# Kernel optimization log

Hardware: AMD Instinct MI355X
Metric: run time of the kernel (lower is better)

## Reference

```python
import jax, jax.numpy as jnp
import numpy as np

K = 3            # kernel_size
PAD = K // 2
CENTER_OFFSET = 0.0


def obb2offset(obb, stride):
    """obb: [N,5,H,W] (x_ctr,y_ctr,w,h,theta) in image coords -> deform offsets [N,2*K*K,H,W]."""
    N, _, H, W = obb.shape
    idx = jnp.arange(-PAD, PAD + 1, dtype=jnp.float32)
    yy, xx = jnp.meshgrid(idx, idx, indexing='ij')   # torch.meshgrid default 'ij'
    xx = xx.reshape(-1)                               # [KK]
    yy = yy.reshape(-1)
    x_ctr, y_ctr, w, h, a = [obb[:, i] for i in range(5)]   # each [N,H,W]
    s = jnp.float32(stride)
    x_ctr, y_ctr, w, h = x_ctr / s, y_ctr / s, w / s, h / s
    cos, sin = jnp.cos(a), jnp.sin(a)
    dw, dh = w / K, h / K
    px = dw[..., None] * xx                           # [N,H,W,KK]
    py = dh[..., None] * yy
    xr = cos[..., None] * px - sin[..., None] * py    # rotate kernel grid by theta
    yr = sin[..., None] * px + cos[..., None] * py
    x_anchor = xr + x_ctr[..., None]
    y_anchor = yr + y_ctr[..., None]
    xc = jnp.arange(W, dtype=jnp.float32)
    yc = jnp.arange(H, dtype=jnp.float32)
    x_conv = xc[None, None, :, None] + xx + CENTER_OFFSET   # [1,1,W,KK]
    y_conv = yc[None, :, None, None] + yy + CENTER_OFFSET   # [1,H,1,KK]
    off = jnp.stack([y_anchor - y_conv, x_anchor - x_conv], axis=-1)  # [N,H,W,KK,2]
    return off.reshape(N, H, W, 2 * K * K).transpose(0, 3, 1, 2)


def deform_conv(x, offsets, weight):
    """Deformable conv v1, zero padding, stride 1. x:[N,Cin,H,W], offsets:[N,2KK,H,W], weight:[Cout,Cin,K,K]."""
    N, Cin, H, W = x.shape
    KK = K * K
    Cout = weight.shape[0]
    off = offsets.reshape(N, KK, 2, H, W)
    dy, dx = off[:, :, 0], off[:, :, 1]                        # [N,KK,H,W]
    ky = jnp.arange(KK, dtype=jnp.float32) // K - PAD
    kx = jnp.arange(KK, dtype=jnp.float32) % K - PAD
    py = jnp.arange(H, dtype=jnp.float32)[None, None, :, None] + ky[None, :, None, None] + dy
    px = jnp.arange(W, dtype=jnp.float32)[None, None, None, :] + kx[None, :, None, None] + dx
    y0 = jnp.floor(py)
    x0 = jnp.floor(px)
    ly = py - y0                                               # bilinear fractions
    lx = px - x0
    y0i = y0.astype(jnp.int32)
    x0i = x0.astype(jnp.int32)
    x_flat = x.reshape(N, Cin, H * W)

    def corner(iy, ix):
        valid = (iy >= 0) & (iy < H) & (ix >= 0) & (ix < W)
        idx = jnp.clip(iy, 0, H - 1) * W + jnp.clip(ix, 0, W - 1)  # [N,KK,H,W]
        g = jax.vmap(lambda xf, ii: xf[:, ii.reshape(-1)].reshape(Cin, KK, H, W))(x_flat, idx)
        return jnp.where(valid[:, None], g, 0.0)               # [N,Cin,KK,H,W]

    v00 = corner(y0i, x0i)
    v01 = corner(y0i, x0i + 1)
    v10 = corner(y0i + 1, x0i)
    v11 = corner(y0i + 1, x0i + 1)
    wy = ly[:, None]
    wx = lx[:, None]
    sampled = (v00 * (1 - wy) * (1 - wx) + v01 * (1 - wy) * wx
               + v10 * wy * (1 - wx) + v11 * wy * wx)          # [N,Cin,KK,H,W]
    return jnp.einsum('nckhw,ock->nohw', sampled, weight.reshape(Cout, Cin, KK))


def setup_inputs() -> dict:
    key = jax.random.key(0)
    k1, k2, k3, k4, k5, k6 = jax.random.split(key, 6)
    N, Cin, Cout, H, W, stride = 2, 256, 256, 128, 128, 8
    x = jax.random.normal(k1, (N, Cin, H, W), jnp.float32)
    gy, gx = jnp.meshgrid(jnp.arange(H, dtype=jnp.float32), jnp.arange(W, dtype=jnp.float32), indexing='ij')
    xc = (gx[None] + jax.random.uniform(k2, (N, H, W), minval=-0.5, maxval=0.5)) * stride
    yc = (gy[None] + jax.random.uniform(k3, (N, H, W), minval=-0.5, maxval=0.5)) * stride
    wb = jax.random.uniform(k4, (N, H, W), minval=2.0 * stride, maxval=8.0 * stride)
    hb = jax.random.uniform(k5, (N, H, W), minval=2.0 * stride, maxval=8.0 * stride)
    th = jax.random.uniform(k6, (N, H, W), minval=-np.pi / 2, maxval=np.pi / 2)
    obb = jnp.stack([xc, yc, wb, hb, th], axis=1)              # [N,5,H,W]
    weight = jax.random.normal(jax.random.fold_in(key, 7), (Cout, Cin, K, K), jnp.float32) * 0.02
    return {"x": x, "obb": obb, "weight": weight, "stride": stride}


def reference(x, obb, weight, stride):
    offsets = obb2offset(jax.lax.stop_gradient(obb), stride)   # offsets.detach() in original
    return deform_conv(x, offsets, weight)
```

## Files before the change

### kernel.cpp

```cpp
#include <hip/hip_runtime.h>

#define HH 128
#define WW 128
#define CIN 256
#define COUT 256
#define KTOT 2304
#define HW (HH * WW)
#define NIT 36

typedef __attribute__((ext_vector_type(8))) short short8;
typedef __attribute__((ext_vector_type(4))) float f32x4;
typedef __attribute__((ext_vector_type(2))) float f32x2;

__device__ __forceinline__ unsigned rne_bf16(float f) {
  unsigned u = __float_as_uint(f);
  return (u + 0x7FFFu + ((u >> 16) & 1u)) >> 16;
}
__device__ __forceinline__ unsigned cvt_pk_bf16(float lo, float hi) {
  unsigned r;
  asm("v_cvt_pk_bf16_f32 %0, %1, %2" : "=v"(r) : "v"(lo), "v"(hi));
  return r;
}
__device__ __forceinline__ f32x2 up2(unsigned u) {
  f32x2 r;
  r.x = __uint_as_float(u << 16);
  r.y = __uint_as_float(u & 0xFFFF0000u);
  return r;
}
__device__ __forceinline__ f32x2 pkmul(f32x2 w, f32x2 v) {
  f32x2 d;
  asm("v_pk_mul_f32 %0, %1, %2" : "=v"(d) : "v"(w), "v"(v));
  return d;
}
__device__ __forceinline__ f32x2 pkfma(f32x2 w, f32x2 v, f32x2 c) {
  f32x2 d;
  asm("v_pk_fma_f32 %0, %1, %2, %3" : "=v"(d) : "v"(w), "v"(v), "v"(c));
  return d;
}

__device__ __forceinline__ void glds16(const void* g, void* l) {
  __builtin_amdgcn_global_load_lds(
      (const __attribute__((address_space(1))) void*)g,
      (__attribute__((address_space(3))) void*)l, 16, 0, 0);
}

__global__ void prep_inputs(const float* __restrict__ x, const float* __restrict__ wsrc,
                            unsigned short* __restrict__ xt, unsigned short* __restrict__ wT) {
  int b = blockIdx.x;
  __shared__ __align__(16) float tile[64][68];
  int tid = threadIdx.x;
  if (b < 2048) {
    int wg = b & 1, cg = (b >> 1) & 3, nh = b >> 3;
    int n = nh >> 7, h = nh & 127;
    const float* xp = x + (((size_t)n * CIN + cg * 64) * HH + h) * WW + wg * 64;
#pragma unroll
    for (int r = 0; r < 4; ++r) {
      int e = r * 256 + tid;
      int ci = e >> 4, w4 = (e & 15) * 4;
      float4 v = *(const float4*)(xp + (size_t)ci * HW + w4);
      tile[w4 + 0][ci] = v.x;
      tile[w4 + 1][ci] = v.y;
      tile[w4 + 2][ci] = v.z;
      tile[w4 + 3][ci] = v.w;
    }
    __syncthreads();
    unsigned short* dst = xt + (((size_t)(n * HH + h) * WW) + wg * 64) * CIN + cg * 64;
#pragma unroll
    for (int r = 0; r < 2; ++r) {
      int e = r * 256 + tid;
      int w = e >> 3, c8 = (e & 7) * 8;
      const float* tp = &tile[w][c8];
      f32x4 lo = *(const f32x4*)tp;
      f32x4 hi = *(const f32x4*)(tp + 4);
      uint4 o;
      o.x = cvt_pk_bf16(lo.x, lo.y);
      o.y = cvt_pk_bf16(lo.z, lo.w);
      o.z = cvt_pk_bf16(hi.x, hi.y);
      o.w = cvt_pk_bf16(hi.z, hi.w);
      *(uint4*)(dst + (size_t)w * CIN + c8) = o;
    }
  } else {
    int o = (b - 2048) * 512 + tid * 2;
    if (o >= COUT * KTOT) return;
    int co = o / KTOT;
    int r = o - co * KTOT;
    int kk = r >> 8, ci = r & 255;
    float v0 = wsrc[(size_t)(co * CIN + ci) * 9 + kk];
    float v1 = wsrc[(size_t)(co * CIN + ci + 1) * 9 + kk];
    *(unsigned*)(wT + o) = cvt_pk_bf16(v0, v1);
  }
}

__global__ __launch_bounds__(512, 2) void fused_deform_gemm(
    const float* __restrict__ obb, const unsigned short* __restrict__ xt,
    const unsigned short* __restrict__ wT, float* __restrict__ out,
    const int* __restrict__ stride_p) {
  int g = blockIdx.x;
  int xcd = g & 7, li = g >> 3;
  int u = xcd * 64 + li;
  int mh = u & 1;
  int bm = u >> 1;
  int n = bm >> 7, h = bm & 127;
  int tid = threadIdx.x;

  __shared__ __align__(16) unsigned short Alds[2][64 * 64];
  __shared__ __align__(16) unsigned short Blds[2][256 * 64];

  float inv_s = 1.0f / (float)stride_p[0];

  int lane = tid & 63;
  int wv = tid >> 6;
  int wm = (wv & 1) * 32;
  int wn = (wv >> 1) * 64;
  int l15 = lane & 15, l4 = lane >> 4;

  int chunk8 = (lane & 7) * 8;
  int p = wv * 8 + (lane >> 3);
  int AldsOff = p * 128 + (((lane & 7) * 16) ^ ((p & 7) << 4));

  int cbl = ((lane & 7) * 16) ^ (((lane >> 3) & 7) << 4);
  const char* wTb = (const char*)wT + (wv * 8 + (lane >> 3)) * (KTOT * 2) + cbl;
  int BldsC[4];
#pragma unroll
  for (int t = 0; t < 4; ++t) BldsC[t] = (t * 64 + wv * 8) * 128;

  float cx_, cy_, pa_, pb_, pc_, pd_;
  {
    int w = mh * 64 + p;
    const float* op = obb + ((size_t)n * 5 * HH + h) * WW + w;
    float xc = op[0] * inv_s;
    float yc = op[(size_t)1 * HW] * inv_s;
    float bw = op[(size_t)2 * HW] * inv_s;
    float bh = op[(size_t)3 * HW] * inv_s;
    float th = op[(size_t)4 * HW];
    float sn, cs;
    sincosf(th, &sn, &cs);
    float dw = bw * (1.0f / 3.0f), dh = bh * (1.0f / 3.0f);
    cx_ = xc; cy_ = yc;
    pa_ = dw * cs; pb_ = dh * sn;
    pc_ = dw * sn; pd_ = dh * cs;
  }

  f32x4 acc[2][4] = {};

  int rdXor = (l15 & 7) << 4;
  int rc0 = (l4 * 16) ^ rdXor;
  int rc1 = (64 + l4 * 16) ^ rdXor;

  f32x2 wgt2[4];
  int boff[4];
  uint4 pf[4];
  uint4 aw;

  auto prep = [&](int kk) {
    float fky = (float)(kk / 3 - 1);
    float fkx = (float)(kk % 3 - 1);
    float sx = cx_ + fkx * pa_ - fky * pb_;
    float sy = cy_ + fkx * pc_ + fky * pd_;
    float fx = floorf(sx), fy = floorf(sy);
    float lx = sx - fx, ly = sy - fy;
    int x0 = (int)fx, y0 = (int)fy;
    float vy0 = (y0 >= 0 && y0 < HH) ? 1.0f : 0.0f;
    float vy1 = (y0 >= -1 && y0 < HH - 1) ? 1.0f : 0.0f;
    float vx0 = (x0 >= 0 && x0 < WW) ? 1.0f : 0.0f;
    float vx1 = (x0 >= -1 && x0 < WW - 1) ? 1.0f : 0.0f;
    float w00 = (1.0f - ly) * (1.0f - lx) * vy0 * vx0;
    float w01 = (1.0f - ly) * lx * vy0 * vx1;
    float w10 = ly * (1.0f - lx) * vy1 * vx0;
    float w11 = ly * lx * vy1 * vx1;
    wgt2[0] = (f32x2){w00, w00};
    wgt2[1] = (f32x2){w01, w01};
    wgt2[2] = (f32x2){w10, w10};
    wgt2[3] = (f32x2){w11, w11};
    int xc0 = min(max(x0, 0), WW - 1), xc1 = min(max(x0 + 1, 0), WW - 1);
    int yc0 = min(max(y0, 0), HH - 1), yc1 = min(max(y0 + 1, 0), HH - 1);
    int rb0 = (n * HH + yc0) * WW, rb1 = (n * HH + yc1) * WW;
    boff[0] = (rb0 + xc0) * CIN;
    boff[1] = (rb0 + xc1) * CIN;
    boff[2] = (rb1 + xc0) * CIN;
    boff[3] = (rb1 + xc1) * CIN;
  };

  auto issueA = [&](int cc) {
    int co = cc * 64 + chunk8;
#pragma unroll
    for (int c = 0; c < 4; ++c)
      pf[c] = *(const uint4*)(xt + boff[c] + co);
  };

  auto blendW = [&](unsigned a, unsigned b, unsigned c, unsigned d) -> unsigned {
    f32x2 s = pkmul(wgt2[0], up2(a));
    s = pkfma(wgt2[1], up2(b), s);
    s = pkfma(wgt2[2], up2(c), s);
    s = pkfma(wgt2[3], up2(d), s);
    return cvt_pk_bf16(s.x, s.y);
  };

  auto blendA = [&]() {
    uint4 r;
    r.x = blendW(pf[0].x, pf[1].x, pf[2].x, pf[3].x);
    r.y = blendW(pf[0].y, pf[1].y, pf[2].y, pf[3].y);
    r.z = blendW(pf[0].z, pf[1].z, pf[2].z, pf[3].z);
    r.w = blendW(pf[0].w, pf[1].w, pf[2].w, pf[3].w);
    aw = r;
  };

  char* AB = (char*)&Alds[0][0];
  char* BB = (char*)&Blds[0][0];

  auto stageB = [&](int itn, int nbuf) {
    const char* src = wTb + itn * 128;
    char* Bd = BB + nbuf * 32768;
#pragma unroll
    for (int t = 0; t < 4; ++t)
      glds16(src + t * (64 * KTOT * 2), Bd + BldsC[t]);
  };

  prep(0);
  issueA(0);
  blendA();
  *(uint4*)(AB + AldsOff) = aw;
  stageB(0, 0);
  issueA(1);
  asm volatile("s_waitcnt vmcnt(4) lgkmcnt(0)" ::: "memory");
  __builtin_amdgcn_s_barrier();
  asm volatile("" ::: "memory");

  for (int it = 0; it < NIT; ++it) {
    int buf = it & 1, nbuf = buf ^ 1;

    if (it + 1 < NIT) {
      blendA();
      *(uint4*)(AB + nbuf * 8192 + AldsOff) = aw;
      stageB(it + 1, nbuf);
      int t2 = it + 2;
      if (t2 < NIT) {
        if ((t2 & 3) == 0) prep(t2 >> 2);
        issueA(t2 & 3);
      }
    }

    char* ABr = AB + buf * 8192;
    char* BBr = BB + buf * 32768;
    __builtin_amdgcn_s_setprio(1);
#pragma unroll
    for (int ksi = 0; ksi < 2; ++ksi) {
      int rc = ksi ? rc1 : rc0;
      short8 af0 = *(const short8*)(ABr + (wm + l15) * 128 + rc);
      short8 af1 = *(const short8*)(ABr + (wm + 16 + l15) * 128 + rc);
#pragma unroll
      for (int j = 0; j < 4; ++j) {
        short8 bf = *(const short8*)(BBr + (wn + j * 16 + l15) * 128 + rc);
        acc[0][j] = __builtin_amdgcn_mfma_f32_16x16x32_bf16(af0, bf, acc[0][j], 0, 0, 0);
        acc[1][j] = __builtin_amdgcn_mfma_f32_16x16x32_bf16(af1, bf, acc[1][j], 0, 0, 0);
      }
    }
    __builtin_amdgcn_s_setprio(0);

    if (it + 1 < NIT) {
      if (it + 2 < NIT) {
        asm volatile("s_waitcnt vmcnt(4) lgkmcnt(0)" ::: "memory");
      } else {
        asm volatile("s_waitcnt vmcnt(0) lgkmcnt(0)" ::: "memory");
      }
      __builtin_amdgcn_s_barrier();
      asm volatile("" ::: "memory");
    }
  }

  float* outp = out + (size_t)n * COUT * HW + (size_t)h * WW + mh * 64;
#pragma unroll
  for (int i = 0; i < 2; ++i) {
    int w0 = wm + i * 16 + l4 * 4;
#pragma unroll
    for (int j = 0; j < 4; ++j) {
      int co = wn + j * 16 + l15;
      *(f32x4*)(outp + (size_t)co * HW + w0) = acc[i][j];
    }
  }
}

extern "C" void kernel_launch(void* const* d_in, const int* in_sizes, int n_in,
                              void* d_out, int out_size, void* d_ws, size_t ws_size,
                              hipStream_t stream) {
  const float* x = (const float*)d_in[0];
  const float* obb = (const float*)d_in[1];
  const float* wgt = (const float*)d_in[2];
  const int* stridep = (const int*)d_in[3];
  float* out = (float*)d_out;

  unsigned short* xt = (unsigned short*)d_ws;
  unsigned short* wT = xt + (size_t)2 * HH * WW * CIN;

  prep_inputs<<<dim3(2048 + 1152), 256, 0, stream>>>(x, wgt, xt, wT);
  fused_deform_gemm<<<dim3(512), 512, 0, stream>>>(obb, xt, wT, out, stridep);
}
```

Measured before the change: 153.6 us.

## Split workgroup into producer and consumer waves for gather and MFMA

Waves 4-7 now act only as producers: they gather the bilinear samples, blend them into the A tile in LDS and stage the weight tiles. Waves 0-3 act only as consumers, each computing a 64x64 output tile with MFMA from LDS. This is meant to overlap the latency-bound gather with tensor-core work across wave specialisation. In exchange, only half the waves do MFMA, consumers hold twice the accumulators, and producers carry twice the prefetch registers.

```diff
diff --git a/kernel.cpp b/kernel.cpp
--- a/kernel.cpp
+++ b/kernel.cpp
@@ -106,26 +106,32 @@
   __shared__ __align__(16) unsigned short Alds[2][64 * 64];
   __shared__ __align__(16) unsigned short Blds[2][256 * 64];
 
-  float inv_s = 1.0f / (float)stride_p[0];
-
   int lane = tid & 63;
   int wv = tid >> 6;
-  int wm = (wv & 1) * 32;
-  int wn = (wv >> 1) * 64;
+  bool isProd = (wv >= 4);
   int l15 = lane & 15, l4 = lane >> 4;
 
-  int chunk8 = (lane & 7) * 8;
-  int p = wv * 8 + (lane >> 3);
-  int AldsOff = p * 128 + (((lane & 7) * 16) ^ ((p & 7) << 4));
-
+  char* AB = (char*)&Alds[0][0];
+  char* BB = (char*)&Blds[0][0];
+
+  int wn = wv * 64;
+  int rdXor = (l15 & 7) << 4;
+  int rc0 = (l4 * 16) ^ rdXor;
+  int rc1 = (64 + l4 * 16) ^ rdXor;
+  f32x4 acc[4][4] = {};
+
+  int pv = wv - 4;
+  int pt = tid & 255;
+  int p = pt >> 2;
+  int chunk4 = pt & 3;
+  int AldsOff0 = p * 128 + ((chunk4 * 32) ^ ((p & 7) << 4));
+  int AldsOff1 = p * 128 + ((chunk4 * 32 + 16) ^ ((p & 7) << 4));
   int cbl = ((lane & 7) * 16) ^ (((lane >> 3) & 7) << 4);
-  const char* wTb = (const char*)wT + (wv * 8 + (lane >> 3)) * (KTOT * 2) + cbl;
-  int BldsC[4];
-#pragma unroll
-  for (int t = 0; t < 4; ++t) BldsC[t] = (t * 64 + wv * 8) * 128;
+  const char* wTb = (const char*)wT + (pv * 8 + (lane >> 3)) * (KTOT * 2) + cbl;
 
   float cx_, cy_, pa_, pb_, pc_, pd_;
-  {
+  if (isProd) {
+    float inv_s = 1.0f / (float)stride_p[0];
     int w = mh * 64 + p;
     const float* op = obb + ((size_t)n * 5 * HH + h) * WW + w;
     float xc = op[0] * inv_s;
@@ -141,16 +147,10 @@
     pc_ = dw * sn; pd_ = dh * cs;
   }
 
-  f32x4 acc[2][4] = {};
-
-  int rdXor = (l15 & 7) << 4;
-  int rc0 = (l4 * 16) ^ rdXor;
-  int rc1 = (64 + l4 * 16) ^ rdXor;
-
   f32x2 wgt2[4];
   int boff[4];
-  uint4 pf[4];
-  uint4 aw;
+  uint4 pf0[4], pf1[4];
+  uint4 aw0, aw1;
 
   auto prep = [&](int kk) {
     float fky = (float)(kk / 3 - 1);
@@ -182,10 +182,12 @@
   };
 
   auto issueA = [&](int cc) {
-    int co = cc * 64 + chunk8;
-#pragma unroll
-    for (int c = 0; c < 4; ++c)
-      pf[c] = *(const uint4*)(xt + boff[c] + co);
+    int co = cc * 64 + chunk4 * 16;
+#pragma unroll
+    for (int c = 0; c < 4; ++c) {
+      pf0[c] = *(const uint4*)(xt + boff[c] + co);
+      pf1[c] = *(const uint4*)(xt + boff[c] + co + 8);
+    }
   };
 
   auto blendW = [&](unsigned a, unsigned b, unsigned c, unsigned d) -> unsigned {
@@ -198,84 +200,96 @@
 
   auto blendA = [&]() {
     uint4 r;
-    r.x = blendW(pf[0].x, pf[1].x, pf[2].x, pf[3].x);
-    r.y = blendW(pf[0].y, pf[1].y, pf[2].y, pf[3].y);
-    r.z = blendW(pf[0].z, pf[1].z, pf[2].z, pf[3].z);
-    r.w = blendW(pf[0].w, pf[1].w, pf[2].w, pf[3].w);
-    aw = r;
-  };
-
-  char* AB = (char*)&Alds[0][0];
-  char* BB = (char*)&Blds[0][0];
+    r.x = blendW(pf0[0].x, pf0[1].x, pf0[2].x, pf0[3].x);
+    r.y = blendW(pf0[0].y, pf0[1].y, pf0[2].y, pf0[3].y);
+    r.z = blendW(pf0[0].z, pf0[1].z, pf0[2].z, pf0[3].z);
+    r.w = blendW(pf0[0].w, pf0[1].w, pf0[2].w, pf0[3].w);
+    aw0 = r;
+    r.x = blendW(pf1[0].x, pf1[1].x, pf1[2].x, pf1[3].x);
+    r.y = blendW(pf1[0].y, pf1[1].y, pf1[2].y, pf1[3].y);
+    r.z = blendW(pf1[0].z, pf1[1].z, pf1[2].z, pf1[3].z);
+    r.w = blendW(pf1[0].w, pf1[1].w, pf1[2].w, pf1[3].w);
+    aw1 = r;
+  };
 
   auto stageB = [&](int itn, int nbuf) {
     const char* src = wTb + itn * 128;
     char* Bd = BB + nbuf * 32768;
 #pragma unroll
-    for (int t = 0; t < 4; ++t)
-      glds16(src + t * (64 * KTOT * 2), Bd + BldsC[t]);
-  };
-
-  prep(0);
-  issueA(0);
-  blendA();
-  *(uint4*)(AB + AldsOff) = aw;
-  stageB(0, 0);
-  issueA(1);
-  asm volatile("s_waitcnt vmcnt(4) lgkmcnt(0)" ::: "memory");
+    for (int t = 0; t < 8; ++t)
+      glds16(src + t * (32 * KTOT * 2), Bd + (t * 32 + pv * 8) * 128);
+  };
+
+  if (isProd) {
+    prep(0);
+    issueA(0);
+    blendA();
+    *(uint4*)(AB + AldsOff0) = aw0;
+    *(uint4*)(AB + AldsOff1) = aw1;
+    stageB(0, 0);
+    issueA(1);
+    asm volatile("s_waitcnt vmcnt(8) lgkmcnt(0)" ::: "memory");
+  }
   __builtin_amdgcn_s_barrier();
   asm volatile("" ::: "memory");
 
   for (int it = 0; it < NIT; ++it) {
     int buf = it & 1, nbuf = buf ^ 1;
 
+    if (isProd) {
+      if (it + 1 < NIT) {
+        stageB(it + 1, nbuf);
+        blendA();
+        *(uint4*)(AB + nbuf * 8192 + AldsOff0) = aw0;
+        *(uint4*)(AB + nbuf * 8192 + AldsOff1) = aw1;
+        int t2 = it + 2;
+        if (t2 < NIT) {
+          if ((t2 & 3) == 0) prep(t2 >> 2);
+          issueA(t2 & 3);
+          asm volatile("s_waitcnt vmcnt(8) lgkmcnt(0)" ::: "memory");
+        } else {
+          asm volatile("s_waitcnt vmcnt(0) lgkmcnt(0)" ::: "memory");
+        }
+      }
+    } else {
+      char* ABr = AB + buf * 8192;
+      char* BBr = BB + buf * 32768;
+      __builtin_amdgcn_s_setprio(1);
+#pragma unroll
+      for (int ksi = 0; ksi < 2; ++ksi) {
+        int rc = ksi ? rc1 : rc0;
+        short8 af[4];
+#pragma unroll
+        for (int i = 0; i < 4; ++i)
+          af[i] = *(const short8*)(ABr + (i * 16 + l15) * 128 + rc);
+#pragma unroll
+        for (int j = 0; j < 4; ++j) {
+          short8 bf = *(const short8*)(BBr + (wn + j * 16 + l15) * 128 + rc);
+#pragma unroll
+          for (int i = 0; i < 4; ++i)
+            acc[i][j] = __builtin_amdgcn_mfma_f32_16x16x32_bf16(af[i], bf, acc[i][j], 0, 0, 0);
+        }
+      }
+      __builtin_amdgcn_s_setprio(0);
+      asm volatile("s_waitcnt lgkmcnt(0)" ::: "memory");
+    }
+
     if (it + 1 < NIT) {
-      blendA();
-      *(uint4*)(AB + nbuf * 8192 + AldsOff) = aw;
-      stageB(it + 1, nbuf);
-      int t2 = it + 2;
-      if (t2 < NIT) {
-        if ((t2 & 3) == 0) prep(t2 >> 2);
-        issueA(t2 & 3);
-      }
-    }
-
-    char* ABr = AB + buf * 8192;
-    char* BBr = BB + buf * 32768;
-    __builtin_amdgcn_s_setprio(1);
-#pragma unroll
-    for (int ksi = 0; ksi < 2; ++ksi) {
-      int rc = ksi ? rc1 : rc0;
-      short8 af0 = *(const short8*)(ABr + (wm + l15) * 128 + rc);
-      short8 af1 = *(const short8*)(ABr + (wm + 16 + l15) * 128 + rc);
-#pragma unroll
-      for (int j = 0; j < 4; ++j) {
-        short8 bf = *(const short8*)(BBr + (wn + j * 16 + l15) * 128 + rc);
-        acc[0][j] = __builtin_amdgcn_mfma_f32_16x16x32_bf16(af0, bf, acc[0][j], 0, 0, 0);
-        acc[1][j] = __builtin_amdgcn_mfma_f32_16x16x32_bf16(af1, bf, acc[1][j], 0, 0, 0);
-      }
-    }
-    __builtin_amdgcn_s_setprio(0);
-
-    if (it + 1 < NIT) {
-      if (it + 2 < NIT) {
-        asm volatile("s_waitcnt vmcnt(4) lgkmcnt(0)" ::: "memory");
-      } else {
-        asm volatile("s_waitcnt vmcnt(0) lgkmcnt(0)" ::: "memory");
-      }
       __builtin_amdgcn_s_barrier();
       asm volatile("" ::: "memory");
     }
   }
 
-  float* outp = out + (size_t)n * COUT * HW + (size_t)h * WW + mh * 64;
-#pragma unroll
-  for (int i = 0; i < 2; ++i) {
-    int w0 = wm + i * 16 + l4 * 4;
-#pragma unroll
-    for (int j = 0; j < 4; ++j) {
-      int co = wn + j * 16 + l15;
-      *(f32x4*)(outp + (size_t)co * HW + w0) = acc[i][j];
+  if (!isProd) {
+    float* outp = out + (size_t)n * COUT * HW + (size_t)h * WW + mh * 64;
+#pragma unroll
+    for (int i = 0; i < 4; ++i) {
+      int w0 = i * 16 + l4 * 4;
+#pragma unroll
+      for (int j = 0; j < 4; ++j) {
+        int co = wn + j * 16 + l15;
+        *(f32x4*)(outp + (size_t)co * HW + w0) = acc[i][j];
+      }
     }
   }
 }
```

New measurement: 176.5 us. 14.9% more time.

## Single-buffer LDS tiles and raise occupancy to four blocks per CU

Applied to the files above, without the earlier changes.

Replaces the double-buffered A/B shared-memory tiles with single buffers, halving LDS use to about 40KB per block, and raises launch bounds so four 512-thread blocks can be resident per CU. Each iteration now writes A, stages B, waits on all outstanding loads with a barrier, computes, then barriers again. The aim is to hide latency through more resident waves instead of software pipelining. In exchange the weight loads are fully exposed within each block, there are two barriers per iteration, and the tighter register budget may cause spills.

```diff
diff --git a/kernel.cpp b/kernel.cpp
--- a/kernel.cpp
+++ b/kernel.cpp
@@ -91,7 +91,7 @@
   }
 }
 
-__global__ __launch_bounds__(512, 2) void fused_deform_gemm(
+__global__ __launch_bounds__(512, 4) void fused_deform_gemm(
     const float* __restrict__ obb, const unsigned short* __restrict__ xt,
     const unsigned short* __restrict__ wT, float* __restrict__ out,
     const int* __restrict__ stride_p) {
@@ -103,10 +103,8 @@
   int n = bm >> 7, h = bm & 127;
   int tid = threadIdx.x;
 
-  __shared__ __align__(16) unsigned short Alds[2][64 * 64];
-  __shared__ __align__(16) unsigned short Blds[2][256 * 64];
-
-  float inv_s = 1.0f / (float)stride_p[0];
+  __shared__ __align__(16) unsigned short Alds[64 * 64];
+  __shared__ __align__(16) unsigned short Blds[256 * 64];
 
   int lane = tid & 63;
   int wv = tid >> 6;
@@ -126,6 +124,7 @@
 
   float cx_, cy_, pa_, pb_, pc_, pd_;
   {
+    float inv_s = 1.0f / (float)stride_p[0];
     int w = mh * 64 + p;
     const float* op = obb + ((size_t)n * 5 * HH + h) * WW + w;
     float xc = op[0] * inv_s;
@@ -205,67 +204,57 @@
     aw = r;
   };
 
-  char* AB = (char*)&Alds[0][0];
-  char* BB = (char*)&Blds[0][0];
-
-  auto stageB = [&](int itn, int nbuf) {
-    const char* src = wTb + itn * 128;
-    char* Bd = BB + nbuf * 32768;
-#pragma unroll
-    for (int t = 0; t < 4; ++t)
-      glds16(src + t * (64 * KTOT * 2), Bd + BldsC[t]);
-  };
+  char* AB = (char*)&Alds[0];
+  char* BB = (char*)&Blds[0];
 
   prep(0);
   issueA(0);
   blendA();
-  *(uint4*)(AB + AldsOff) = aw;
-  stageB(0, 0);
   issueA(1);
-  asm volatile("s_waitcnt vmcnt(4) lgkmcnt(0)" ::: "memory");
-  __builtin_amdgcn_s_barrier();
-  asm volatile("" ::: "memory");
 
   for (int it = 0; it < NIT; ++it) {
-    int buf = it & 1, nbuf = buf ^ 1;
-
-    if (it + 1 < NIT) {
+    *(uint4*)(AB + AldsOff) = aw;
+    {
+      const char* src = wTb + it * 128;
+#pragma unroll
+      for (int t = 0; t < 4; ++t)
+        glds16(src + t * (64 * KTOT * 2), BB + BldsC[t]);
+    }
+    asm volatile("s_waitcnt vmcnt(0) lgkmcnt(0)" ::: "memory");
+    __builtin_amdgcn_s_barrier();
+    asm volatile("" ::: "memory");
+
+    int nx = it + 1;
+    if (nx < NIT) {
       blendA();
-      *(uint4*)(AB + nbuf * 8192 + AldsOff) = aw;
-      stageB(it + 1, nbuf);
-      int t2 = it + 2;
-      if (t2 < NIT) {
-        if ((t2 & 3) == 0) prep(t2 >> 2);
-        issueA(t2 & 3);
+      int nn = it + 2;
+      if (nn < NIT) {
+        if ((nn & 3) == 0) prep(nn >> 2);
+        issueA(nn & 3);
       }
     }
 
-    char* ABr = AB + buf * 8192;
-    char* BBr = BB + buf * 32768;
     __builtin_amdgcn_s_setprio(1);
 #pragma unroll
     for (int ksi = 0; ksi < 2; ++ksi) {
       int rc = ksi ? rc1 : rc0;
-      short8 af0 = *(const short8*)(ABr + (wm + l15) * 128 + rc);
-      short8 af1 = *(const short8*)(ABr + (wm + 16 + l15) * 128 + rc);
+      short8 af[2];
+#pragma unroll
+      for (int i = 0; i < 2; ++i)
+        af[i] = *(const short8*)(AB + (wm + i * 16 + l15) * 128 + rc);
 #pragma unroll
       for (int j = 0; j < 4; ++j) {
-        short8 bf = *(const short8*)(BBr + (wn + j * 16 + l15) * 128 + rc);
-        acc[0][j] = __builtin_amdgcn_mfma_f32_16x16x32_bf16(af0, bf, acc[0][j], 0, 0, 0);
-        acc[1][j] = __builtin_amdgcn_mfma_f32_16x16x32_bf16(af1, bf, acc[1][j], 0, 0, 0);
+        short8 bf = *(const short8*)(BB + (wn + j * 16 + l15) * 128 + rc);
+#pragma unroll
+        for (int i = 0; i < 2; ++i)
+          acc[i][j] = __builtin_amdgcn_mfma_f32_16x16x32_bf16(af[i], bf, acc[i][j], 0, 0, 0);
       }
     }
     __builtin_amdgcn_s_setprio(0);
 
-    if (it + 1 < NIT) {
-      if (it + 2 < NIT) {
-        asm volatile("s_waitcnt vmcnt(4) lgkmcnt(0)" ::: "memory");
-      } else {
-        asm volatile("s_waitcnt vmcnt(0) lgkmcnt(0)" ::: "memory");
-      }
-      __builtin_amdgcn_s_barrier();
-      asm volatile("" ::: "memory");
-    }
+    asm volatile("s_waitcnt lgkmcnt(0)" ::: "memory");
+    __builtin_amdgcn_s_barrier();
+    asm volatile("" ::: "memory");
   }
 
   float* outp = out + (size_t)n * COUT * HW + (size_t)h * WW + mh * 64;
```

After: 159.2 us. 1.04x slower.
